# Performance work log

Hardware: AMD Instinct MI355X
Metric: run time of the kernel (lower is better)

The kernel has to match this reference:

```python
import jax, jax.numpy as jnp
import numpy as np

C = 4        # num_case (3) + coreference (1)
H = 128      # self.hidden_size
D = 768      # bert hidden size
B, S = 2, 384


def setup_inputs() -> dict:
    key = jax.random.key(0)
    ks = jax.random.split(key, 9)
    sc = 0.02
    return {
        "sequence_output": jax.random.normal(ks[0], (B, S, D), jnp.float32),
        "base_score": jax.random.uniform(ks[1], (B, S, C, S), jnp.float32),
        "W_prd_w": jax.random.normal(ks[2], (D, C * H), jnp.float32) * sc,
        "W_prd_b": jnp.zeros((C * H,), jnp.float32),
        "U_arg_w": jax.random.normal(ks[3], (D, C * H), jnp.float32) * sc,
        "U_arg_b": jnp.zeros((C * H,), jnp.float32),
        "W_mid": jax.random.normal(ks[4], (H * (C + 2), H), jnp.float32) * sc,
        "b_mid": jnp.zeros((H,), jnp.float32),
        "w_out": jax.random.normal(ks[5], (H,), jnp.float32) * sc,
    }


def reference(sequence_output, base_score, W_prd_w, W_prd_b, U_arg_w, U_arg_b, W_mid, b_mid, w_out):
    b, s, _ = sequence_output.shape
    # projections (dropout = identity in eval)
    h_p = (sequence_output @ W_prd_w + W_prd_b).reshape(b, s, C, H)   # [B,S,C,H]
    h_a = (sequence_output @ U_arg_w + U_arg_b).reshape(b, s, C, H)   # [B,S,C,H]
    # weighted_sum over argument positions: base_score[b,prd,case,arg]
    ref = jnp.einsum("bach,bpca->bpch", h_a, base_score).reshape(b, s, C * H)  # [B,S,C*H]
    # mid_layer(tanh(cat[prd_rep, h_a, ref])) == sum of three block matmuls,
    # since tanh is elementwise on each concatenated block.
    W1, W2, W3 = W_mid[:H], W_mid[H:2 * H], W_mid[2 * H:]
    t_prd = jnp.einsum("bpch,hk->bpck", jnp.tanh(h_p), W1)   # [B,Sp,C,H]
    t_arg = jnp.einsum("bach,hk->back", jnp.tanh(h_a), W2)   # [B,Sa,C,H]
    t_ref = jnp.tanh(ref) @ W3                                # [B,Sp,H]
    h_mid = (t_prd[:, :, None, :, :] + t_arg[:, None, :, :, :]
             + t_ref[:, :, None, None, :] + b_mid)            # [B,Sp,Sa,C,H]
    out = jnp.tanh(h_mid) @ w_out                             # [B,Sp,Sa,C]
    return out.transpose(0, 1, 3, 2)                          # [B,Sp,C,Sa]
```

## Files before the change

kernel.cpp:

```cpp
#include <hip/hip_runtime.h>
#include <hip/hip_bf16.h>


#define C2 2.885390081777927f

typedef __attribute__((ext_vector_type(8))) __bf16 bf16x8;
typedef __attribute__((ext_vector_type(8))) unsigned short ushort8;
typedef __attribute__((ext_vector_type(4))) float float4v;

__device__ __forceinline__ unsigned short f2bf(float f) {
  unsigned int u = __float_as_uint(f);
  u += 0x7fffu + ((u >> 16) & 1u);
  return (unsigned short)(u >> 16);
}

__device__ __forceinline__ float fast_tanh(float x) {
  float e = __builtin_amdgcn_exp2f(C2 * x);
  return 1.0f - 2.0f * __builtin_amdgcn_rcpf(1.0f + e);
}

__device__ __forceinline__ void gemm_core(
    const float* __restrict__ Abase, int lda,
    const float* __restrict__ Bbase, int ldb, int K,
    unsigned short* Alds, unsigned short* Blds,
    int ar, int ac, int bk, int bn,
    int wm0, int wn0, int col16, int quad, float4v acc[2][2])
{
  const float* Ap = Abase + (size_t)ar * lda + ac;
  const float* Bp = Bbase + (size_t)bk * ldb + bn;
  float4 a0 = ((const float4*)Ap)[0], a1 = ((const float4*)Ap)[1];
  float4 b0 = ((const float4*)Bp)[0], b1 = ((const float4*)Bp)[1];

  for (int k0 = 0; k0 < K; k0 += 32) {
    __syncthreads();
    {
      ushort8 o;
      o[0] = f2bf(a0.x); o[1] = f2bf(a0.y); o[2] = f2bf(a0.z); o[3] = f2bf(a0.w);
      o[4] = f2bf(a1.x); o[5] = f2bf(a1.y); o[6] = f2bf(a1.z); o[7] = f2bf(a1.w);
      *(ushort8*)&Alds[ar * 40 + ac] = o;
      float vv[8] = {b0.x, b0.y, b0.z, b0.w, b1.x, b1.y, b1.z, b1.w};
#pragma unroll
      for (int j = 0; j < 8; ++j) Blds[(bn + j) * 40 + bk] = f2bf(vv[j]);
    }
    __syncthreads();
    if (k0 + 32 < K) {
      const float4* An = (const float4*)(Ap + k0 + 32);
      const float4* Bn = (const float4*)(Bp + (size_t)(k0 + 32) * ldb);
      a0 = An[0]; a1 = An[1]; b0 = Bn[0]; b1 = Bn[1];
    }
    bf16x8 afrag[2], bfrag[2];
#pragma unroll
    for (int i = 0; i < 2; ++i)
      afrag[i] = __builtin_bit_cast(bf16x8,
          *(const ushort8*)&Alds[(wm0 + i * 16 + col16) * 40 + quad * 8]);
#pragma unroll
    for (int j = 0; j < 2; ++j)
      bfrag[j] = __builtin_bit_cast(bf16x8,
          *(const ushort8*)&Blds[(wn0 + j * 16 + col16) * 40 + quad * 8]);
#pragma unroll
    for (int i = 0; i < 2; ++i)
#pragma unroll
      for (int j = 0; j < 2; ++j)
        acc[i][j] = __builtin_amdgcn_mfma_f32_16x16x32_bf16(
            afrag[i], bfrag[j], acc[i][j], 0, 0, 0);
  }
}

__global__ __launch_bounds__(256) void g1_dual(
    const float* __restrict__ seq, const float* __restrict__ Wp,
    const float* __restrict__ Ua, const float* __restrict__ Wpb,
    const float* __restrict__ Uab, float* __restrict__ tanh_out,
    float* __restrict__ h_a, float* __restrict__ tref_clear)
{
  const int z = blockIdx.z;
  if (z == 2) {
    int idx = ((blockIdx.y * 8 + blockIdx.x) * 256 + threadIdx.x) * 4;
    *(float4*)&tref_clear[idx] = float4{0.f, 0.f, 0.f, 0.f};
    return;
  }
  __shared__ unsigned short Alds[64 * 40];
  __shared__ unsigned short Blds[64 * 40];
  const int tid = threadIdx.x;
  const int bn0 = blockIdx.x * 64, bm0 = blockIdx.y * 64;
  const int wid = tid >> 6, lane = tid & 63;
  const int wm0 = (wid >> 1) * 32, wn0 = (wid & 1) * 32;
  const int col16 = lane & 15, quad = lane >> 4;
  const float* B = z ? Ua : Wp;
  const float* bias = z ? Uab : Wpb;

  float4v acc[2][2];
#pragma unroll
  for (int i = 0; i < 2; ++i)
#pragma unroll
    for (int j = 0; j < 2; ++j) acc[i][j] = (float4v)(0.f);

  gemm_core(seq + (size_t)bm0 * 768, 768, B + bn0, 512, 768,
            Alds, Blds, tid >> 2, (tid & 3) * 8, tid >> 3, (tid & 7) * 8,
            wm0, wn0, col16, quad, acc);

  float* tout = tanh_out + (size_t)z * 393216;
#pragma unroll
  for (int j = 0; j < 2; ++j) {
    const int gcol = bn0 + wn0 + j * 16 + col16;
    const float bv = bias[gcol];
#pragma unroll
    for (int i = 0; i < 2; ++i)
#pragma unroll
      for (int r = 0; r < 4; ++r) {
        const int grow = bm0 + wm0 + i * 16 + quad * 4 + r;
        const float x = acc[i][j][r] + bv;
        const size_t cidx = (size_t)grow * 512 + gcol;
        tout[cidx] = fast_tanh(x);
        if (z == 1) h_a[cidx] = x;
      }
  }
}

__global__ __launch_bounds__(256) void fused_mid(
    const float* __restrict__ base, const float* __restrict__ h_a,
    const float* __restrict__ tanh_h, const float* __restrict__ Wmid,
    float* __restrict__ tprd_s, unsigned short* __restrict__ targ_s,
    float* __restrict__ tref_s)
{
  __shared__ unsigned short Alds[64 * 40];
  __shared__ unsigned short Blds[64 * 40];
  __shared__ unsigned short TA[64 * 72];
  __shared__ unsigned short TB[128 * 72];

  const int tid = threadIdx.x;
  const int bid = blockIdx.x;
  const int wid = tid >> 6, lane = tid & 63;
  const int wm0 = (wid >> 1) * 32, wn0 = (wid & 1) * 32;
  const int col16 = lane & 15, quad = lane >> 4;
  const int ar = tid >> 2, ac = (tid & 3) * 8;
  const int bk = tid >> 3, bn = (tid & 7) * 8;

  float4v acc[2][2];
#pragma unroll
  for (int i = 0; i < 2; ++i)
#pragma unroll
    for (int j = 0; j < 2; ++j) acc[i][j] = (float4v)(0.f);

  if (bid < 96) {
    const int z = bid / 12, rem = bid % 12;
    const int b = z >> 2, c = z & 3;
    const int y = rem >> 1, x = rem & 1;
    const float* A = base + (size_t)b * 589824 + c * 384 + (size_t)(y * 64) * 1536;
    const float* Bm = h_a + (size_t)b * 196608 + c * 128 + x * 64;
    gemm_core(A, 1536, Bm, 512, 384, Alds, Blds, ar, ac, bk, bn,
              wm0, wn0, col16, quad, acc);

#pragma unroll
    for (int j = 0; j < 2; ++j)
#pragma unroll
      for (int i = 0; i < 2; ++i)
#pragma unroll
        for (int r = 0; r < 4; ++r)
          TA[(wm0 + i * 16 + quad * 4 + r) * 72 + wn0 + j * 16 + col16] =
              f2bf(fast_tanh(acc[i][j][r]));
    {
      const float* W3p = Wmid + 32768 + (size_t)(c * 128 + x * 64) * 128;
      const int kr = tid >> 2, nb = (tid & 3) * 32;
#pragma unroll
      for (int q = 0; q < 8; ++q) {
        float4 v = *(const float4*)(W3p + (size_t)kr * 128 + nb + q * 4);
        TB[(nb + q * 4 + 0) * 72 + kr] = f2bf(v.x);
        TB[(nb + q * 4 + 1) * 72 + kr] = f2bf(v.y);
        TB[(nb + q * 4 + 2) * 72 + kr] = f2bf(v.z);
        TB[(nb + q * 4 + 3) * 72 + kr] = f2bf(v.w);
      }
    }
    __syncthreads();

    const int mh = wid & 1, nh = wid >> 1;
    float4v acc2[2][4];
#pragma unroll
    for (int i = 0; i < 2; ++i)
#pragma unroll
      for (int j = 0; j < 4; ++j) acc2[i][j] = (float4v)(0.f);
#pragma unroll
    for (int ks = 0; ks < 2; ++ks) {
      bf16x8 af[2], bf[4];
#pragma unroll
      for (int i = 0; i < 2; ++i)
        af[i] = __builtin_bit_cast(bf16x8,
            *(const ushort8*)&TA[(mh * 32 + i * 16 + col16) * 72 + ks * 32 + quad * 8]);
#pragma unroll
      for (int j = 0; j < 4; ++j)
        bf[j] = __builtin_bit_cast(bf16x8,
            *(const ushort8*)&TB[(nh * 64 + j * 16 + col16) * 72 + ks * 32 + quad * 8]);
#pragma unroll
      for (int i = 0; i < 2; ++i)
#pragma unroll
        for (int j = 0; j < 4; ++j)
          acc2[i][j] = __builtin_amdgcn_mfma_f32_16x16x32_bf16(
              af[i], bf[j], acc2[i][j], 0, 0, 0);
    }
#pragma unroll
    for (int j = 0; j < 4; ++j) {
      const int gcol = nh * 64 + j * 16 + col16;
#pragma unroll
      for (int i = 0; i < 2; ++i)
#pragma unroll
        for (int r = 0; r < 4; ++r) {
          const int grow = b * 384 + y * 64 + mh * 32 + i * 16 + quad * 4 + r;
          atomicAdd(&tref_s[(size_t)grow * 128 + gcol], C2 * acc2[i][j][r]);
        }
    }
  } else {
    const int idx = bid - 96;
    const int x = idx & 1, y = (idx >> 1) % 48, z = idx / 96;
    const float* A = tanh_h + (size_t)z * 393216 + (size_t)(y * 64) * 128;
    const float* Bm = Wmid + z * 16384 + x * 64;
    gemm_core(A, 128, Bm, 128, 128, Alds, Blds, ar, ac, bk, bn,
              wm0, wn0, col16, quad, acc);
#pragma unroll
    for (int j = 0; j < 2; ++j) {
      const int gcol = x * 64 + wn0 + j * 16 + col16;
#pragma unroll
      for (int i = 0; i < 2; ++i)
#pragma unroll
        for (int r = 0; r < 4; ++r) {
          const int grow = y * 64 + wm0 + i * 16 + quad * 4 + r;
          const float v = C2 * acc[i][j][r];
          const size_t cidx = (size_t)grow * 128 + gcol;
          if (z == 0) tprd_s[cidx] = v;
          else        targ_s[cidx] = f2bf(v);
        }
    }
  }
}

__global__ __launch_bounds__(128) void phase2(
    const float* __restrict__ tprd, const unsigned short* __restrict__ targ,
    const float* __restrict__ tref, const float* __restrict__ bmid,
    const float* __restrict__ wout, float* __restrict__ out)
{
  __shared__ unsigned int Gs[128 * 34];
  __shared__ float Es[8 * 128];
  __shared__ float Ws[128];

  const int tid = threadIdx.x;
  const int p0 = blockIdx.x * 8, a0 = blockIdx.y * 128;
  const int b = blockIdx.z >> 2, c = blockIdx.z & 3;

  if (tid < 32) {
    float4 w = ((const float4*)wout)[tid];
    Ws[tid * 4 + 0] = -2.f * w.x; Ws[tid * 4 + 1] = -2.f * w.y;
    Ws[tid * 4 + 2] = -2.f * w.z; Ws[tid * 4 + 3] = -2.f * w.w;
  }
#pragma unroll
  for (int it = 0; it < 8; ++it) {
    int idx = it * 128 + tid;
    int p = idx >> 7, k = idx & 127;
    int row = b * 384 + p0 + p;
    float f = tprd[(size_t)(row * 4 + c) * 128 + k] +
              tref[(size_t)row * 128 + k] + C2 * bmid[k];
    Es[idx] = __builtin_amdgcn_exp2f(f);
  }
  float sw = 0.f;
  for (int k4 = 0; k4 < 32; ++k4) {
    float4 w = ((const float4*)wout)[k4];
    sw += w.x + w.y + w.z + w.w;
  }

  float acc01[8], acc23[8];
#pragma unroll
  for (int p = 0; p < 8; ++p) { acc01[p] = 0.f; acc23[p] = 0.f; }

  const unsigned int* gsrc = (const unsigned int*)targ;
  const size_t grow_base = (size_t)((b * 384 + a0) * 4 + c) * 64;

  for (int h = 0; h < 2; ++h) {
    __syncthreads();
#pragma unroll 8
    for (int it = 0; it < 32; ++it) {
      int idx = it * 128 + tid;
      int r = idx >> 5, col = idx & 31;
      Gs[r * 34 + col] = gsrc[grow_base + (size_t)r * 256 + h * 32 + col];
    }
    __syncthreads();

    const unsigned int* g = &Gs[tid * 34];
    const int kb = h * 64;
#pragma unroll 2
    for (int j = 0; j < 16; ++j) {
      uint2 gp = *(const uint2*)(g + j * 2);
      float eg0 = __builtin_amdgcn_exp2f(__uint_as_float(gp.x << 16));
      float eg1 = __builtin_amdgcn_exp2f(__uint_as_float(gp.x & 0xffff0000u));
      float eg2 = __builtin_amdgcn_exp2f(__uint_as_float(gp.y << 16));
      float eg3 = __builtin_amdgcn_exp2f(__uint_as_float(gp.y & 0xffff0000u));
      float4 wq = *(const float4*)&Ws[kb + j * 4];
#pragma unroll
      for (int p = 0; p < 8; ++p) {
        float4 ef = *(const float4*)&Es[p * 128 + kb + j * 4];
        float d0 = fmaf(ef.x, eg0, 1.f);
        float d1 = fmaf(ef.y, eg1, 1.f);
        float d2 = fmaf(ef.z, eg2, 1.f);
        float d3 = fmaf(ef.w, eg3, 1.f);
        float r01 = __builtin_amdgcn_rcpf(d0 * d1);
        float r23 = __builtin_amdgcn_rcpf(d2 * d3);
        float n01 = fmaf(wq.y, d0, wq.x * d1);
        float n23 = fmaf(wq.w, d2, wq.z * d3);
        acc01[p] = fmaf(n01, r01, acc01[p]);
        acc23[p] = fmaf(n23, r23, acc23[p]);
      }
    }
  }

  const size_t ob = (size_t)((b * 384 + p0) * 4 + c) * 384 + a0 + tid;
#pragma unroll
  for (int p = 0; p < 8; ++p)
    out[ob + (size_t)p * 1536] = sw + acc01[p] + acc23[p];
}

extern "C" void kernel_launch(void* const* d_in, const int* in_sizes, int n_in,
                              void* d_out, int out_size, void* d_ws, size_t ws_size,
                              hipStream_t stream) {
  (void)in_sizes; (void)n_in; (void)out_size; (void)ws_size;
  const float* seq  = (const float*)d_in[0];
  const float* base = (const float*)d_in[1];
  const float* Wp   = (const float*)d_in[2];
  const float* Wpb  = (const float*)d_in[3];
  const float* Ua   = (const float*)d_in[4];
  const float* Uab  = (const float*)d_in[5];
  const float* Wmid = (const float*)d_in[6];
  const float* bmid = (const float*)d_in[7];
  const float* wout = (const float*)d_in[8];
  float* out = (float*)d_out;

  float* ws = (float*)d_ws;
  float* tanh_hp = ws;
  float* h_a     = ws + 786432;
  float* tprd_s  = ws + 1179648;
  float* tref_s  = ws + 1572864;
  unsigned short* targ_s = (unsigned short*)(ws + 1671168);

  g1_dual<<<dim3(8, 12, 3), dim3(256), 0, stream>>>(
      seq, Wp, Ua, Wpb, Uab, tanh_hp, h_a, tref_s);
  fused_mid<<<dim3(288), dim3(256), 0, stream>>>(
      base, h_a, tanh_hp, Wmid, tprd_s, targ_s, tref_s);
  phase2<<<dim3(48, 3, 8), dim3(128), 0, stream>>>(
      tprd_s, targ_s, tref_s, bmid, wout, out);
}
```

Measured before the change: 140.5 us.

## Merge three kernels into one persistent kernel with software grid barriers

Replaces the three separate launches (projection GEMM, mid GEMMs, pairwise tanh-reduction) with one 512-block kernel. The stages are separated by atomic-counter grid barriers, and LDS is shared across stages through a single buffer. The final stage is redistributed as evenly split jobs per block, with the K dimension split across two thread halves and reduced through LDS. It also merges the per-element reciprocals so one rcp covers four terms. This aims to remove inter-kernel launch gaps and tail effects, but it relies on all blocks being co-resident. The barrier reset/gate on bar[0] may also be racy across repeated launches, since the MAGIC value from an earlier call persists.

```diff
diff --git a/kernel.cpp b/kernel.cpp
--- a/kernel.cpp
+++ b/kernel.cpp
@@ -3,6 +3,8 @@
 
 
 #define C2 2.885390081777927f
+#define NBLK 512
+#define MAGIC 0x13579BDFu
 
 typedef __attribute__((ext_vector_type(8))) __bf16 bf16x8;
 typedef __attribute__((ext_vector_type(8))) unsigned short ushort8;
@@ -66,66 +68,48 @@
   }
 }
 
-__global__ __launch_bounds__(256) void g1_dual(
-    const float* __restrict__ seq, const float* __restrict__ Wp,
-    const float* __restrict__ Ua, const float* __restrict__ Wpb,
-    const float* __restrict__ Uab, float* __restrict__ tanh_out,
-    float* __restrict__ h_a, float* __restrict__ tref_clear)
+__device__ __forceinline__ void grid_barrier(unsigned* cnt, unsigned* rel,
+                                             int bid) {
+  __syncthreads();
+  if (threadIdx.x == 0) {
+    __hip_atomic_fetch_add(&cnt[(bid & 7) * 32], 1u, __ATOMIC_ACQ_REL,
+                           __HIP_MEMORY_SCOPE_AGENT);
+    if (bid == 0) {
+      for (long g = 0; g < (1L << 24); ++g) {
+        unsigned s = 0;
+#pragma unroll
+        for (int i = 0; i < 8; ++i)
+          s += __hip_atomic_load(&cnt[i * 32], __ATOMIC_ACQUIRE,
+                                 __HIP_MEMORY_SCOPE_AGENT);
+        if (s == NBLK) break;
+        __builtin_amdgcn_s_sleep(2);
+      }
+      __hip_atomic_store(rel, MAGIC, __ATOMIC_RELEASE,
+                         __HIP_MEMORY_SCOPE_AGENT);
+    } else {
+      for (long g = 0; g < (1L << 24); ++g) {
+        if (__hip_atomic_load(rel, __ATOMIC_ACQUIRE,
+                              __HIP_MEMORY_SCOPE_AGENT) == MAGIC) break;
+        __builtin_amdgcn_s_sleep(2);
+      }
+    }
+  }
+  __syncthreads();
+}
+
+__global__ __launch_bounds__(256, 4) void mono(
+    const float* __restrict__ seq, const float* __restrict__ base,
+    const float* __restrict__ Wp, const float* __restrict__ Wpb,
+    const float* __restrict__ Ua, const float* __restrict__ Uab,
+    const float* __restrict__ Wmid, const float* __restrict__ bmid,
+    const float* __restrict__ wout, float* __restrict__ out,
+    float* __restrict__ tanh_h, float* __restrict__ h_a,
+    float* __restrict__ tprd_s, float* __restrict__ tref_s,
+    unsigned short* __restrict__ targ_s, unsigned* __restrict__ bar)
 {
-  const int z = blockIdx.z;
-  if (z == 2) {
-    int idx = ((blockIdx.y * 8 + blockIdx.x) * 256 + threadIdx.x) * 4;
-    *(float4*)&tref_clear[idx] = float4{0.f, 0.f, 0.f, 0.f};
-    return;
-  }
-  __shared__ unsigned short Alds[64 * 40];
-  __shared__ unsigned short Blds[64 * 40];
-  const int tid = threadIdx.x;
-  const int bn0 = blockIdx.x * 64, bm0 = blockIdx.y * 64;
-  const int wid = tid >> 6, lane = tid & 63;
-  const int wm0 = (wid >> 1) * 32, wn0 = (wid & 1) * 32;
-  const int col16 = lane & 15, quad = lane >> 4;
-  const float* B = z ? Ua : Wp;
-  const float* bias = z ? Uab : Wpb;
-
-  float4v acc[2][2];
-#pragma unroll
-  for (int i = 0; i < 2; ++i)
-#pragma unroll
-    for (int j = 0; j < 2; ++j) acc[i][j] = (float4v)(0.f);
-
-  gemm_core(seq + (size_t)bm0 * 768, 768, B + bn0, 512, 768,
-            Alds, Blds, tid >> 2, (tid & 3) * 8, tid >> 3, (tid & 7) * 8,
-            wm0, wn0, col16, quad, acc);
-
-  float* tout = tanh_out + (size_t)z * 393216;
-#pragma unroll
-  for (int j = 0; j < 2; ++j) {
-    const int gcol = bn0 + wn0 + j * 16 + col16;
-    const float bv = bias[gcol];
-#pragma unroll
-    for (int i = 0; i < 2; ++i)
-#pragma unroll
-      for (int r = 0; r < 4; ++r) {
-        const int grow = bm0 + wm0 + i * 16 + quad * 4 + r;
-        const float x = acc[i][j][r] + bv;
-        const size_t cidx = (size_t)grow * 512 + gcol;
-        tout[cidx] = fast_tanh(x);
-        if (z == 1) h_a[cidx] = x;
-      }
-  }
-}
-
-__global__ __launch_bounds__(256) void fused_mid(
-    const float* __restrict__ base, const float* __restrict__ h_a,
-    const float* __restrict__ tanh_h, const float* __restrict__ Wmid,
-    float* __restrict__ tprd_s, unsigned short* __restrict__ targ_s,
-    float* __restrict__ tref_s)
-{
-  __shared__ unsigned short Alds[64 * 40];
-  __shared__ unsigned short Blds[64 * 40];
-  __shared__ unsigned short TA[64 * 72];
-  __shared__ unsigned short TB[128 * 72];
+  __shared__ __align__(16) unsigned char smem[28672];
+  unsigned short* Alds = (unsigned short*)smem;
+  unsigned short* Blds = (unsigned short*)(smem + 5120);
 
   const int tid = threadIdx.x;
   const int bid = blockIdx.x;
@@ -135,183 +119,249 @@
   const int ar = tid >> 2, ac = (tid & 3) * 8;
   const int bk = tid >> 3, bn = (tid & 7) * 8;
 
-  float4v acc[2][2];
-#pragma unroll
-  for (int i = 0; i < 2; ++i)
-#pragma unroll
-    for (int j = 0; j < 2; ++j) acc[i][j] = (float4v)(0.f);
-
-  if (bid < 96) {
-    const int z = bid / 12, rem = bid % 12;
-    const int b = z >> 2, c = z & 3;
-    const int y = rem >> 1, x = rem & 1;
-    const float* A = base + (size_t)b * 589824 + c * 384 + (size_t)(y * 64) * 1536;
-    const float* Bm = h_a + (size_t)b * 196608 + c * 128 + x * 64;
-    gemm_core(A, 1536, Bm, 512, 384, Alds, Blds, ar, ac, bk, bn,
-              wm0, wn0, col16, quad, acc);
-
-#pragma unroll
-    for (int j = 0; j < 2; ++j)
+  if (bid == 0 && tid == 0) {
+#pragma unroll
+    for (int i = 0; i < 8; ++i) {
+      __hip_atomic_store(&bar[32 + i * 32], 0u, __ATOMIC_RELAXED,
+                         __HIP_MEMORY_SCOPE_AGENT);
+      __hip_atomic_store(&bar[512 + i * 32], 0u, __ATOMIC_RELAXED,
+                         __HIP_MEMORY_SCOPE_AGENT);
+    }
+    __hip_atomic_store(&bar[16], 0u, __ATOMIC_RELAXED, __HIP_MEMORY_SCOPE_AGENT);
+    __hip_atomic_store(&bar[24], 0u, __ATOMIC_RELAXED, __HIP_MEMORY_SCOPE_AGENT);
+    __hip_atomic_store(&bar[0], MAGIC, __ATOMIC_RELEASE,
+                       __HIP_MEMORY_SCOPE_AGENT);
+  }
+
+  if (bid < 192) {
+    const int z = bid / 96, rem = bid % 96;
+    const int bn0 = (rem & 7) * 64, bm0 = (rem >> 3) * 64;
+    const float* Bm = (z ? Ua : Wp) + bn0;
+    const float* bias = z ? Uab : Wpb;
+    float4v acc[2][2];
+#pragma unroll
+    for (int i = 0; i < 2; ++i)
+#pragma unroll
+      for (int j = 0; j < 2; ++j) acc[i][j] = (float4v)(0.f);
+    gemm_core(seq + (size_t)bm0 * 768, 768, Bm, 512, 768,
+              Alds, Blds, ar, ac, bk, bn, wm0, wn0, col16, quad, acc);
+    float* tout = tanh_h + (size_t)z * 393216;
+#pragma unroll
+    for (int j = 0; j < 2; ++j) {
+      const int gcol = bn0 + wn0 + j * 16 + col16;
+      const float bv = bias[gcol];
 #pragma unroll
       for (int i = 0; i < 2; ++i)
 #pragma unroll
-        for (int r = 0; r < 4; ++r)
-          TA[(wm0 + i * 16 + quad * 4 + r) * 72 + wn0 + j * 16 + col16] =
-              f2bf(fast_tanh(acc[i][j][r]));
-    {
-      const float* W3p = Wmid + 32768 + (size_t)(c * 128 + x * 64) * 128;
-      const int kr = tid >> 2, nb = (tid & 3) * 32;
-#pragma unroll
-      for (int q = 0; q < 8; ++q) {
-        float4 v = *(const float4*)(W3p + (size_t)kr * 128 + nb + q * 4);
-        TB[(nb + q * 4 + 0) * 72 + kr] = f2bf(v.x);
-        TB[(nb + q * 4 + 1) * 72 + kr] = f2bf(v.y);
-        TB[(nb + q * 4 + 2) * 72 + kr] = f2bf(v.z);
-        TB[(nb + q * 4 + 3) * 72 + kr] = f2bf(v.w);
-      }
-    }
-    __syncthreads();
-
-    const int mh = wid & 1, nh = wid >> 1;
-    float4v acc2[2][4];
+        for (int r = 0; r < 4; ++r) {
+          const int grow = bm0 + wm0 + i * 16 + quad * 4 + r;
+          const float x = acc[i][j][r] + bv;
+          const size_t cidx = (size_t)grow * 512 + gcol;
+          tout[cidx] = fast_tanh(x);
+          if (z == 1) h_a[cidx] = x;
+        }
+    }
+  } else {
+    for (int idx = (bid - 192) * 256 + tid; idx < 98304; idx += 81920)
+      tref_s[idx] = 0.f;
+  }
+
+  if (tid == 0) {
+    for (long g = 0; g < (1L << 24); ++g) {
+      if (__hip_atomic_load(&bar[0], __ATOMIC_ACQUIRE,
+                            __HIP_MEMORY_SCOPE_AGENT) == MAGIC) break;
+      __builtin_amdgcn_s_sleep(2);
+    }
+  }
+  grid_barrier(&bar[32], &bar[16], bid);
+
+  if (bid < 288) {
+    float4v acc[2][2];
 #pragma unroll
     for (int i = 0; i < 2; ++i)
 #pragma unroll
-      for (int j = 0; j < 4; ++j) acc2[i][j] = (float4v)(0.f);
-#pragma unroll
-    for (int ks = 0; ks < 2; ++ks) {
-      bf16x8 af[2], bf[4];
+      for (int j = 0; j < 2; ++j) acc[i][j] = (float4v)(0.f);
+
+    if (bid < 96) {
+      unsigned short* TA = (unsigned short*)smem;
+      unsigned short* TB = (unsigned short*)(smem + 9216);
+      const int z = bid / 12, rem = bid % 12;
+      const int b = z >> 2, c = z & 3;
+      const int y = rem >> 1, x = rem & 1;
+      const float* A = base + (size_t)b * 589824 + c * 384 + (size_t)(y * 64) * 1536;
+      const float* Bm = h_a + (size_t)b * 196608 + c * 128 + x * 64;
+      gemm_core(A, 1536, Bm, 512, 384, Alds, Blds, ar, ac, bk, bn,
+                wm0, wn0, col16, quad, acc);
+      __syncthreads();
+#pragma unroll
+      for (int j = 0; j < 2; ++j)
+#pragma unroll
+        for (int i = 0; i < 2; ++i)
+#pragma unroll
+          for (int r = 0; r < 4; ++r)
+            TA[(wm0 + i * 16 + quad * 4 + r) * 72 + wn0 + j * 16 + col16] =
+                f2bf(fast_tanh(acc[i][j][r]));
+      {
+        const float* W3p = Wmid + 32768 + (size_t)(c * 128 + x * 64) * 128;
+        const int kr = tid >> 2, nb = (tid & 3) * 32;
+#pragma unroll
+        for (int q = 0; q < 8; ++q) {
+          float4 v = *(const float4*)(W3p + (size_t)kr * 128 + nb + q * 4);
+          TB[(nb + q * 4 + 0) * 72 + kr] = f2bf(v.x);
+          TB[(nb + q * 4 + 1) * 72 + kr] = f2bf(v.y);
+          TB[(nb + q * 4 + 2) * 72 + kr] = f2bf(v.z);
+          TB[(nb + q * 4 + 3) * 72 + kr] = f2bf(v.w);
+        }
+      }
+      __syncthreads();
+      const int mh = wid & 1, nh = wid >> 1;
+      float4v acc2[2][4];
 #pragma unroll
       for (int i = 0; i < 2; ++i)
-        af[i] = __builtin_bit_cast(bf16x8,
-            *(const ushort8*)&TA[(mh * 32 + i * 16 + col16) * 72 + ks * 32 + quad * 8]);
-#pragma unroll
-      for (int j = 0; j < 4; ++j)
-        bf[j] = __builtin_bit_cast(bf16x8,
-            *(const ushort8*)&TB[(nh * 64 + j * 16 + col16) * 72 + ks * 32 + quad * 8]);
-#pragma unroll
-      for (int i = 0; i < 2; ++i)
+#pragma unroll
+        for (int j = 0; j < 4; ++j) acc2[i][j] = (float4v)(0.f);
+#pragma unroll
+      for (int ks = 0; ks < 2; ++ks) {
+        bf16x8 af[2], bf[4];
+#pragma unroll
+        for (int i = 0; i < 2; ++i)
+          af[i] = __builtin_bit_cast(bf16x8,
+              *(const ushort8*)&TA[(mh * 32 + i * 16 + col16) * 72 + ks * 32 + quad * 8]);
 #pragma unroll
         for (int j = 0; j < 4; ++j)
-          acc2[i][j] = __builtin_amdgcn_mfma_f32_16x16x32_bf16(
-              af[i], bf[j], acc2[i][j], 0, 0, 0);
-    }
-#pragma unroll
-    for (int j = 0; j < 4; ++j) {
-      const int gcol = nh * 64 + j * 16 + col16;
-#pragma unroll
-      for (int i = 0; i < 2; ++i)
-#pragma unroll
-        for (int r = 0; r < 4; ++r) {
-          const int grow = b * 384 + y * 64 + mh * 32 + i * 16 + quad * 4 + r;
-          atomicAdd(&tref_s[(size_t)grow * 128 + gcol], C2 * acc2[i][j][r]);
-        }
-    }
-  } else {
-    const int idx = bid - 96;
-    const int x = idx & 1, y = (idx >> 1) % 48, z = idx / 96;
-    const float* A = tanh_h + (size_t)z * 393216 + (size_t)(y * 64) * 128;
-    const float* Bm = Wmid + z * 16384 + x * 64;
-    gemm_core(A, 128, Bm, 128, 128, Alds, Blds, ar, ac, bk, bn,
-              wm0, wn0, col16, quad, acc);
-#pragma unroll
-    for (int j = 0; j < 2; ++j) {
-      const int gcol = x * 64 + wn0 + j * 16 + col16;
-#pragma unroll
-      for (int i = 0; i < 2; ++i)
-#pragma unroll
-        for (int r = 0; r < 4; ++r) {
-          const int grow = y * 64 + wm0 + i * 16 + quad * 4 + r;
-          const float v = C2 * acc[i][j][r];
-          const size_t cidx = (size_t)grow * 128 + gcol;
-          if (z == 0) tprd_s[cidx] = v;
-          else        targ_s[cidx] = f2bf(v);
-        }
-    }
-  }
-}
-
-__global__ __launch_bounds__(128) void phase2(
-    const float* __restrict__ tprd, const unsigned short* __restrict__ targ,
-    const float* __restrict__ tref, const float* __restrict__ bmid,
-    const float* __restrict__ wout, float* __restrict__ out)
-{
-  __shared__ unsigned int Gs[128 * 34];
-  __shared__ float Es[8 * 128];
-  __shared__ float Ws[128];
-
-  const int tid = threadIdx.x;
-  const int p0 = blockIdx.x * 8, a0 = blockIdx.y * 128;
-  const int b = blockIdx.z >> 2, c = blockIdx.z & 3;
-
-  if (tid < 32) {
-    float4 w = ((const float4*)wout)[tid];
-    Ws[tid * 4 + 0] = -2.f * w.x; Ws[tid * 4 + 1] = -2.f * w.y;
-    Ws[tid * 4 + 2] = -2.f * w.z; Ws[tid * 4 + 3] = -2.f * w.w;
-  }
-#pragma unroll
-  for (int it = 0; it < 8; ++it) {
-    int idx = it * 128 + tid;
-    int p = idx >> 7, k = idx & 127;
-    int row = b * 384 + p0 + p;
-    float f = tprd[(size_t)(row * 4 + c) * 128 + k] +
-              tref[(size_t)row * 128 + k] + C2 * bmid[k];
-    Es[idx] = __builtin_amdgcn_exp2f(f);
-  }
+          bf[j] = __builtin_bit_cast(bf16x8,
+              *(const ushort8*)&TB[(nh * 64 + j * 16 + col16) * 72 + ks * 32 + quad * 8]);
+#pragma unroll
+        for (int i = 0; i < 2; ++i)
+#pragma unroll
+          for (int j = 0; j < 4; ++j)
+            acc2[i][j] = __builtin_amdgcn_mfma_f32_16x16x32_bf16(
+                af[i], bf[j], acc2[i][j], 0, 0, 0);
+      }
+#pragma unroll
+      for (int j = 0; j < 4; ++j) {
+        const int gcol = nh * 64 + j * 16 + col16;
+#pragma unroll
+        for (int i = 0; i < 2; ++i)
+#pragma unroll
+          for (int r = 0; r < 4; ++r) {
+            const int grow = b * 384 + y * 64 + mh * 32 + i * 16 + quad * 4 + r;
+            atomicAdd(&tref_s[(size_t)grow * 128 + gcol], C2 * acc2[i][j][r]);
+          }
+      }
+    } else {
+      const int idx = bid - 96;
+      const int x = idx & 1, y = (idx >> 1) % 48, z = idx / 96;
+      const float* A = tanh_h + (size_t)z * 393216 + (size_t)(y * 64) * 128;
+      const float* Bm = Wmid + z * 16384 + x * 64;
+      gemm_core(A, 128, Bm, 128, 128, Alds, Blds, ar, ac, bk, bn,
+                wm0, wn0, col16, quad, acc);
+#pragma unroll
+      for (int j = 0; j < 2; ++j) {
+        const int gcol = x * 64 + wn0 + j * 16 + col16;
+#pragma unroll
+        for (int i = 0; i < 2; ++i)
+#pragma unroll
+          for (int r = 0; r < 4; ++r) {
+            const int grow = y * 64 + wm0 + i * 16 + quad * 4 + r;
+            const float v = C2 * acc[i][j][r];
+            const size_t cidx = (size_t)grow * 128 + gcol;
+            if (z == 0) tprd_s[cidx] = v;
+            else        targ_s[cidx] = f2bf(v);
+          }
+      }
+    }
+  }
+
+  grid_barrier(&bar[512], &bar[24], bid);
+
+  unsigned int* Gs = (unsigned int*)smem;
+  float* Es  = (float*)(smem + 17408);
+  float* Ws  = (float*)(smem + 21504);
+  float* Red = (float*)(smem + 22016);
+
+  if (tid < 128) Ws[tid] = -2.f * wout[tid];
   float sw = 0.f;
   for (int k4 = 0; k4 < 32; ++k4) {
     float4 w = ((const float4*)wout)[k4];
     sw += w.x + w.y + w.z + w.w;
   }
 
-  float acc01[8], acc23[8];
-#pragma unroll
-  for (int p = 0; p < 8; ++p) { acc01[p] = 0.f; acc23[p] = 0.f; }
-
-  const unsigned int* gsrc = (const unsigned int*)targ;
-  const size_t grow_base = (size_t)((b * 384 + a0) * 4 + c) * 64;
-
-  for (int h = 0; h < 2; ++h) {
+  const unsigned int* gsrc = (const unsigned int*)targ_s;
+  const int a = tid & 127, kh = tid >> 7;
+  const int j0 = (bid * 9) >> 2, j1 = ((bid + 1) * 9) >> 2;
+
+  for (int job = j0; job < j1; ++job) {
+    const int s = job / 48, pt = job % 48;
+    const int at = s % 3, zz = s / 3;
+    const int b = zz >> 2, c = zz & 3;
+    const int p0 = pt * 8, a0 = at * 128;
+    const size_t gb = (size_t)((b * 384 + a0) * 4 + c) * 64;
+
     __syncthreads();
-#pragma unroll 8
-    for (int it = 0; it < 32; ++it) {
-      int idx = it * 128 + tid;
-      int r = idx >> 5, col = idx & 31;
-      Gs[r * 34 + col] = gsrc[grow_base + (size_t)r * 256 + h * 32 + col];
+#pragma unroll
+    for (int it = 0; it < 4; ++it) {
+      int idx = it * 256 + tid;
+      int p = idx >> 7, k = idx & 127;
+      int row = b * 384 + p0 + p;
+      Es[idx] = __builtin_amdgcn_exp2f(
+          tprd_s[(size_t)(row * 4 + c) * 128 + k] +
+          tref_s[(size_t)row * 128 + k] + C2 * bmid[k]);
+    }
+
+    float acc[8];
+#pragma unroll
+    for (int p = 0; p < 8; ++p) acc[p] = 0.f;
+
+    for (int h = 0; h < 2; ++h) {
+      if (h) __syncthreads();
+#pragma unroll 4
+      for (int it = 0; it < 16; ++it) {
+        int idx = it * 256 + tid;
+        int r = idx >> 5, col = idx & 31;
+        Gs[r * 34 + col] = gsrc[gb + (size_t)r * 256 + h * 32 + col];
+      }
+      __syncthreads();
+
+      const unsigned int* g = &Gs[a * 34 + kh * 16];
+      const int kb = h * 64 + kh * 32;
+#pragma unroll 2
+      for (int j = 0; j < 8; ++j) {
+        uint2 gp = *(const uint2*)(g + j * 2);
+        float eg0 = __builtin_amdgcn_exp2f(__uint_as_float(gp.x << 16));
+        float eg1 = __builtin_amdgcn_exp2f(__uint_as_float(gp.x & 0xffff0000u));
+        float eg2 = __builtin_amdgcn_exp2f(__uint_as_float(gp.y << 16));
+        float eg3 = __builtin_amdgcn_exp2f(__uint_as_float(gp.y & 0xffff0000u));
+        float4 wq = *(const float4*)&Ws[kb + j * 4];
+#pragma unroll
+        for (int p = 0; p < 8; ++p) {
+          float4 ef = *(const float4*)&Es[p * 128 + kb + j * 4];
+          float d0 = fmaf(ef.x, eg0, 1.f);
+          float d1 = fmaf(ef.y, eg1, 1.f);
+          float d2 = fmaf(ef.z, eg2, 1.f);
+          float d3 = fmaf(ef.w, eg3, 1.f);
+          float d01 = d0 * d1, d23 = d2 * d3;
+          float n01 = fmaf(wq.y, d0, wq.x * d1);
+          float n23 = fmaf(wq.w, d2, wq.z * d3);
+          float num = fmaf(n01, d23, n23 * d01);
+          float r = __builtin_amdgcn_rcpf(d01 * d23);
+          acc[p] = fmaf(num, r, acc[p]);
+        }
+      }
+    }
+
+    if (kh) {
+#pragma unroll
+      for (int p = 0; p < 8; ++p) Red[a * 9 + p] = acc[p];
     }
     __syncthreads();
-
-    const unsigned int* g = &Gs[tid * 34];
-    const int kb = h * 64;
-#pragma unroll 2
-    for (int j = 0; j < 16; ++j) {
-      uint2 gp = *(const uint2*)(g + j * 2);
-      float eg0 = __builtin_amdgcn_exp2f(__uint_as_float(gp.x << 16));
-      float eg1 = __builtin_amdgcn_exp2f(__uint_as_float(gp.x & 0xffff0000u));
-      float eg2 = __builtin_amdgcn_exp2f(__uint_as_float(gp.y << 16));
-      float eg3 = __builtin_amdgcn_exp2f(__uint_as_float(gp.y & 0xffff0000u));
-      float4 wq = *(const float4*)&Ws[kb + j * 4];
-#pragma unroll
-      for (int p = 0; p < 8; ++p) {
-        float4 ef = *(const float4*)&Es[p * 128 + kb + j * 4];
-        float d0 = fmaf(ef.x, eg0, 1.f);
-        float d1 = fmaf(ef.y, eg1, 1.f);
-        float d2 = fmaf(ef.z, eg2, 1.f);
-        float d3 = fmaf(ef.w, eg3, 1.f);
-        float r01 = __builtin_amdgcn_rcpf(d0 * d1);
-        float r23 = __builtin_amdgcn_rcpf(d2 * d3);
-        float n01 = fmaf(wq.y, d0, wq.x * d1);
-        float n23 = fmaf(wq.w, d2, wq.z * d3);
-        acc01[p] = fmaf(n01, r01, acc01[p]);
-        acc23[p] = fmaf(n23, r23, acc23[p]);
-      }
-    }
-  }
-
-  const size_t ob = (size_t)((b * 384 + p0) * 4 + c) * 384 + a0 + tid;
-#pragma unroll
-  for (int p = 0; p < 8; ++p)
-    out[ob + (size_t)p * 1536] = sw + acc01[p] + acc23[p];
+    if (!kh) {
+      const size_t ob = (size_t)((b * 384 + p0) * 4 + c) * 384 + a0 + a;
+#pragma unroll
+      for (int p = 0; p < 8; ++p)
+        out[ob + (size_t)p * 1536] = sw + acc[p] + Red[a * 9 + p];
+    }
+  }
 }
 
 extern "C" void kernel_launch(void* const* d_in, const int* in_sizes, int n_in,
@@ -330,16 +380,14 @@
   float* out = (float*)d_out;
 
   float* ws = (float*)d_ws;
-  float* tanh_hp = ws;
-  float* h_a     = ws + 786432;
-  float* tprd_s  = ws + 1179648;
-  float* tref_s  = ws + 1572864;
+  float* tanh_h = ws;
+  float* h_a    = ws + 786432;
+  float* tprd_s = ws + 1179648;
+  float* tref_s = ws + 1572864;
   unsigned short* targ_s = (unsigned short*)(ws + 1671168);
-
-  g1_dual<<<dim3(8, 12, 3), dim3(256), 0, stream>>>(
-      seq, Wp, Ua, Wpb, Uab, tanh_hp, h_a, tref_s);
-  fused_mid<<<dim3(288), dim3(256), 0, stream>>>(
-      base, h_a, tanh_hp, Wmid, tprd_s, targ_s, tref_s);
-  phase2<<<dim3(48, 3, 8), dim3(128), 0, stream>>>(
-      tprd_s, targ_s, tref_s, bmid, wout, out);
-}
+  unsigned* bar = (unsigned*)((char*)d_ws + (16u << 20));
+
+  mono<<<dim3(NBLK), dim3(256), 0, stream>>>(
+      seq, base, Wp, Wpb, Ua, Uab, Wmid, bmid, wout, out,
+      tanh_h, h_a, tprd_s, tref_s, targ_s, bar);
+}
```

After: 382.4 us. +172.2%, slower.

## Split phase2 K dimension across two thread halves with register-held targ rows

Applied to the files above, without the earlier changes.

phase2 now runs 256 threads per block, and the two halves each handle half of the 128-wide hidden dimension for the same 128 argument columns. The halves' partial sums are combined through shared memory before the store. Each thread loads its targ slice straight into registers as uint4, which removes the LDS staging buffer and its two barriers. The tanh-sum math is also restructured to take one reciprocal per four elements instead of one per two. This adds occupancy and cuts transcendental work, at the cost of a reduction step, more register pressure, and slightly different rounding.

```diff
diff --git a/kernel.cpp b/kernel.cpp
--- a/kernel.cpp
+++ b/kernel.cpp
@@ -231,87 +231,98 @@
   }
 }
 
-__global__ __launch_bounds__(128) void phase2(
+__global__ __launch_bounds__(256) void phase2(
     const float* __restrict__ tprd, const unsigned short* __restrict__ targ,
     const float* __restrict__ tref, const float* __restrict__ bmid,
     const float* __restrict__ wout, float* __restrict__ out)
 {
-  __shared__ unsigned int Gs[128 * 34];
   __shared__ float Es[8 * 128];
   __shared__ float Ws[128];
+  __shared__ float Red[128 * 9];
 
   const int tid = threadIdx.x;
+  const int a = tid & 127, kh = tid >> 7;
   const int p0 = blockIdx.x * 8, a0 = blockIdx.y * 128;
   const int b = blockIdx.z >> 2, c = blockIdx.z & 3;
 
-  if (tid < 32) {
-    float4 w = ((const float4*)wout)[tid];
-    Ws[tid * 4 + 0] = -2.f * w.x; Ws[tid * 4 + 1] = -2.f * w.y;
-    Ws[tid * 4 + 2] = -2.f * w.z; Ws[tid * 4 + 3] = -2.f * w.w;
-  }
-#pragma unroll
-  for (int it = 0; it < 8; ++it) {
-    int idx = it * 128 + tid;
+  const uint4* grow = (const uint4*)((const unsigned int*)targ +
+      (size_t)((b * 384 + a0 + a) * 4 + c) * 64 + kh * 32);
+  uint4 G[8];
+#pragma unroll
+  for (int i = 0; i < 8; ++i) G[i] = grow[i];
+
+  if (tid < 128) Ws[tid] = -2.f * wout[tid];
+#pragma unroll
+  for (int it = 0; it < 4; ++it) {
+    int idx = it * 256 + tid;
     int p = idx >> 7, k = idx & 127;
     int row = b * 384 + p0 + p;
-    float f = tprd[(size_t)(row * 4 + c) * 128 + k] +
-              tref[(size_t)row * 128 + k] + C2 * bmid[k];
-    Es[idx] = __builtin_amdgcn_exp2f(f);
+    Es[idx] = __builtin_amdgcn_exp2f(
+        tprd[(size_t)(row * 4 + c) * 128 + k] +
+        tref[(size_t)row * 128 + k] + C2 * bmid[k]);
   }
   float sw = 0.f;
   for (int k4 = 0; k4 < 32; ++k4) {
     float4 w = ((const float4*)wout)[k4];
     sw += w.x + w.y + w.z + w.w;
   }
-
-  float acc01[8], acc23[8];
-#pragma unroll
-  for (int p = 0; p < 8; ++p) { acc01[p] = 0.f; acc23[p] = 0.f; }
-
-  const unsigned int* gsrc = (const unsigned int*)targ;
-  const size_t grow_base = (size_t)((b * 384 + a0) * 4 + c) * 64;
-
-  for (int h = 0; h < 2; ++h) {
-    __syncthreads();
-#pragma unroll 8
-    for (int it = 0; it < 32; ++it) {
-      int idx = it * 128 + tid;
-      int r = idx >> 5, col = idx & 31;
-      Gs[r * 34 + col] = gsrc[grow_base + (size_t)r * 256 + h * 32 + col];
-    }
-    __syncthreads();
-
-    const unsigned int* g = &Gs[tid * 34];
-    const int kb = h * 64;
-#pragma unroll 2
-    for (int j = 0; j < 16; ++j) {
-      uint2 gp = *(const uint2*)(g + j * 2);
-      float eg0 = __builtin_amdgcn_exp2f(__uint_as_float(gp.x << 16));
-      float eg1 = __builtin_amdgcn_exp2f(__uint_as_float(gp.x & 0xffff0000u));
-      float eg2 = __builtin_amdgcn_exp2f(__uint_as_float(gp.y << 16));
-      float eg3 = __builtin_amdgcn_exp2f(__uint_as_float(gp.y & 0xffff0000u));
-      float4 wq = *(const float4*)&Ws[kb + j * 4];
-#pragma unroll
-      for (int p = 0; p < 8; ++p) {
-        float4 ef = *(const float4*)&Es[p * 128 + kb + j * 4];
-        float d0 = fmaf(ef.x, eg0, 1.f);
-        float d1 = fmaf(ef.y, eg1, 1.f);
-        float d2 = fmaf(ef.z, eg2, 1.f);
-        float d3 = fmaf(ef.w, eg3, 1.f);
-        float r01 = __builtin_amdgcn_rcpf(d0 * d1);
-        float r23 = __builtin_amdgcn_rcpf(d2 * d3);
-        float n01 = fmaf(wq.y, d0, wq.x * d1);
-        float n23 = fmaf(wq.w, d2, wq.z * d3);
-        acc01[p] = fmaf(n01, r01, acc01[p]);
-        acc23[p] = fmaf(n23, r23, acc23[p]);
-      }
-    }
-  }
-
-  const size_t ob = (size_t)((b * 384 + p0) * 4 + c) * 384 + a0 + tid;
-#pragma unroll
-  for (int p = 0; p < 8; ++p)
-    out[ob + (size_t)p * 1536] = sw + acc01[p] + acc23[p];
+  __syncthreads();
+
+  float acc[8];
+#pragma unroll
+  for (int p = 0; p < 8; ++p) acc[p] = 0.f;
+
+  const int kb0 = kh * 64;
+#pragma unroll
+  for (int j = 0; j < 8; ++j) {
+    const uint4 gq = G[j];
+    const float eg0 = __builtin_amdgcn_exp2f(__uint_as_float(gq.x << 16));
+    const float eg1 = __builtin_amdgcn_exp2f(__uint_as_float(gq.x & 0xffff0000u));
+    const float eg2 = __builtin_amdgcn_exp2f(__uint_as_float(gq.y << 16));
+    const float eg3 = __builtin_amdgcn_exp2f(__uint_as_float(gq.y & 0xffff0000u));
+    const float eg4 = __builtin_amdgcn_exp2f(__uint_as_float(gq.z << 16));
+    const float eg5 = __builtin_amdgcn_exp2f(__uint_as_float(gq.z & 0xffff0000u));
+    const float eg6 = __builtin_amdgcn_exp2f(__uint_as_float(gq.w << 16));
+    const float eg7 = __builtin_amdgcn_exp2f(__uint_as_float(gq.w & 0xffff0000u));
+    const int kb = kb0 + j * 8;
+    const float4 wqA = *(const float4*)&Ws[kb];
+    const float4 wqB = *(const float4*)&Ws[kb + 4];
+#pragma unroll
+    for (int p = 0; p < 8; ++p) {
+      const float4 efA = *(const float4*)&Es[p * 128 + kb];
+      const float4 efB = *(const float4*)&Es[p * 128 + kb + 4];
+      float d0 = fmaf(efA.x, eg0, 1.f);
+      float d1 = fmaf(efA.y, eg1, 1.f);
+      float d2 = fmaf(efA.z, eg2, 1.f);
+      float d3 = fmaf(efA.w, eg3, 1.f);
+      float d01 = d0 * d1, d23 = d2 * d3;
+      float n01 = fmaf(wqA.y, d0, wqA.x * d1);
+      float n23 = fmaf(wqA.w, d2, wqA.z * d3);
+      float num = fmaf(n01, d23, n23 * d01);
+      acc[p] = fmaf(num, __builtin_amdgcn_rcpf(d01 * d23), acc[p]);
+      d0 = fmaf(efB.x, eg4, 1.f);
+      d1 = fmaf(efB.y, eg5, 1.f);
+      d2 = fmaf(efB.z, eg6, 1.f);
+      d3 = fmaf(efB.w, eg7, 1.f);
+      d01 = d0 * d1; d23 = d2 * d3;
+      n01 = fmaf(wqB.y, d0, wqB.x * d1);
+      n23 = fmaf(wqB.w, d2, wqB.z * d3);
+      num = fmaf(n01, d23, n23 * d01);
+      acc[p] = fmaf(num, __builtin_amdgcn_rcpf(d01 * d23), acc[p]);
+    }
+  }
+
+  if (kh) {
+#pragma unroll
+    for (int p = 0; p < 8; ++p) Red[a * 9 + p] = acc[p];
+  }
+  __syncthreads();
+  if (!kh) {
+    const size_t ob = (size_t)((b * 384 + p0) * 4 + c) * 384 + a0 + a;
+#pragma unroll
+    for (int p = 0; p < 8; ++p)
+      out[ob + (size_t)p * 1536] = sw + acc[p] + Red[a * 9 + p];
+  }
 }
 
 extern "C" void kernel_launch(void* const* d_in, const int* in_sizes, int n_in,
@@ -330,16 +341,16 @@
   float* out = (float*)d_out;
 
   float* ws = (float*)d_ws;
-  float* tanh_hp = ws;
-  float* h_a     = ws + 786432;
-  float* tprd_s  = ws + 1179648;
-  float* tref_s  = ws + 1572864;
+  float* tanh_h = ws;
+  float* h_a    = ws + 786432;
+  float* tprd_s = ws + 1179648;
+  float* tref_s = ws + 1572864;
   unsigned short* targ_s = (unsigned short*)(ws + 1671168);
 
   g1_dual<<<dim3(8, 12, 3), dim3(256), 0, stream>>>(
-      seq, Wp, Ua, Wpb, Uab, tanh_hp, h_a, tref_s);
+      seq, Wp, Ua, Wpb, Uab, tanh_h, h_a, tref_s);
   fused_mid<<<dim3(288), dim3(256), 0, stream>>>(
-      base, h_a, tanh_hp, Wmid, tprd_s, targ_s, tref_s);
-  phase2<<<dim3(48, 3, 8), dim3(128), 0, stream>>>(
+      base, h_a, tanh_h, Wmid, tprd_s, targ_s, tref_s);
+  phase2<<<dim3(48, 3, 8), dim3(256), 0, stream>>>(
       tprd_s, targ_s, tref_s, bmid, wout, out);
 }
```

Measured after the change: 131.6 us. -6.3%, faster.
